# Kernel tuning notes

Measured on AMD Instinct MI355X. Metric: run time of the kernel, lower is better.

The kernel has to match this reference:

```python
import jax, jax.numpy as jnp
import numpy as np

H_SIZE = 1024
N_HEADS = 16
HEAD_DIM = H_SIZE // N_HEADS
TAU2 = 1.0
LN_EPS = 1e-5


def setup_inputs() -> dict:
    key = jax.random.key(0)
    ks = jax.random.split(key, 12)
    B, S = 2, 1024
    s = 1.0 / np.sqrt(H_SIZE)
    inp = {
        "input": jax.random.normal(ks[0], (B, S, H_SIZE), dtype=jnp.float32),
        "input_mask": jnp.ones((B, S), dtype=jnp.float32),
        # uniform(0,1) noise; converted to Gumbel(0,1) inside reference
        "gumbel": jax.random.uniform(ks[1], (B, N_HEADS, S, S), dtype=jnp.float32,
                                     minval=1e-10, maxval=1.0),
        "Wq": jax.random.normal(ks[2], (H_SIZE, H_SIZE), dtype=jnp.float32) * s,
        "bq": jnp.zeros((H_SIZE,), dtype=jnp.float32),
        "Wk": jax.random.normal(ks[3], (H_SIZE, H_SIZE), dtype=jnp.float32) * s,
        "bk": jnp.zeros((H_SIZE,), dtype=jnp.float32),
        "Wv": jax.random.normal(ks[4], (H_SIZE, H_SIZE), dtype=jnp.float32) * s,
        "bv": jnp.zeros((H_SIZE,), dtype=jnp.float32),
        "Wo": jax.random.normal(ks[5], (H_SIZE, H_SIZE), dtype=jnp.float32) * s,
        "bo": jnp.zeros((H_SIZE,), dtype=jnp.float32),
        "gamma": jnp.ones((H_SIZE,), dtype=jnp.float32),
        "beta": jnp.zeros((H_SIZE,), dtype=jnp.float32),
    }
    return inp


def reference(input, input_mask, gumbel, Wq, bq, Wk, bk, Wv, bv, Wo, bo, gamma, beta):
    B, S, _ = input.shape
    # projections -> [B, H, S, D]
    def proj(W, b):
        y = jnp.einsum('bsh,oh->bso', input, W) + b  # torch Linear: x @ W.T + b
        return y.reshape(B, S, N_HEADS, HEAD_DIM).transpose(0, 2, 1, 3)
    qq = proj(Wq, bq)
    kk = proj(Wk, bk)
    vv = proj(Wv, bv)
    # raw scores (NOTE: original has no 1/sqrt(d) scaling)
    interact = jnp.einsum('bhqd,bhkd->bhqk', qq, kk)
    # gumbel-softmax (soft): softmax((logits + g)/tau)
    g = -jnp.log(-jnp.log(gumbel))
    sto_attn = jax.nn.softmax((interact + g) / TAU2, axis=-1)
    # masking: mask_1 over query dim, mask_2 over key dim
    mask = input_mask[:, None, :, None] * input_mask[:, None, None, :]  # [B,1,S,S]
    attn = sto_attn * mask
    # (dropout p=0 -> identity)
    out = jnp.einsum('bhqk,bhkd->bhqd', attn, vv)
    out = out.transpose(0, 2, 1, 3).reshape(B, S, H_SIZE)
    out = jnp.einsum('bsh,oh->bso', out, Wo) + bo
    # residual + layernorm
    x = out + input
    mu = jnp.mean(x, axis=-1, keepdims=True)
    var = jnp.mean(jnp.square(x - mu), axis=-1, keepdims=True)
    return (x - mu) * jax.lax.rsqrt(var + LN_EPS) * gamma + beta
```

## Files before the change

### kernel.cpp

```cpp
#include <hip/hip_runtime.h>

#define S_LEN 1024
#define HSZ   1024
#define NHEAD 16
#define HD    64
#define BATCH 2
#define MROWS 2048
#define SOFTMAX_M0 50.0f

typedef unsigned short u16;
typedef __attribute__((ext_vector_type(8))) short short8;
typedef __attribute__((ext_vector_type(4))) short short4v;
typedef __attribute__((ext_vector_type(4))) float f32x4;

#define MFMA_BF16(a, b, c) __builtin_amdgcn_mfma_f32_16x16x32_bf16((a), (b), (c), 0, 0, 0)

__device__ __forceinline__ u16 f2bf(float f) {
    union { float f; unsigned u; } c; c.f = f;
    unsigned u = c.u;
    u += 0x7fffu + ((u >> 16) & 1u);
    return (u16)(u >> 16);
}
__device__ __forceinline__ float bf2f(u16 s) {
    union { unsigned u; float f; } c; c.u = ((unsigned)s) << 16;
    return c.f;
}
__device__ __forceinline__ short8 ld8(const u16* p) {
    return *reinterpret_cast<const short8*>(p);
}
__device__ __forceinline__ void gld16(const u16* g, u16* l) {
    __builtin_amdgcn_global_load_lds(
        (const __attribute__((address_space(1))) unsigned int*)g,
        (__attribute__((address_space(3))) unsigned int*)l, 16, 0, 0);
}
__device__ __forceinline__ int frag_off(int row, int cbb) {
    return (((row << 3) | (cbb ^ (row & 7))) << 3);
}

template<int MT>
__device__ __forceinline__ void gemm_tile(const u16* __restrict__ Ag,
                                          const u16* __restrict__ Bg,
                                          int klen, u16* As, u16* Bs,
                                          f32x4 (&acc)[MT][4]) {
    const int tid  = threadIdx.x;
    const int wave = tid >> 6, lane = tid & 63;
    const int lr = lane & 15, grp = lane >> 4;
    const int wm = wave >> 1, wn = wave & 1;

#pragma unroll
    for (int mt = 0; mt < MT; mt++)
#pragma unroll
        for (int nt = 0; nt < 4; nt++)
            acc[mt][nt] = (f32x4){0.f, 0.f, 0.f, 0.f};

    for (int k0 = 0; k0 < klen; k0 += 64) {
        __syncthreads();
#pragma unroll
        for (int j = 0; j < MT; j++) {
            int c = j * 256 + tid, row = c >> 3, cb = (c & 7) ^ (row & 7);
            gld16(Ag + (size_t)row * HSZ + k0 + cb * 8, As + c * 8);
        }
#pragma unroll
        for (int j = 0; j < 4; j++) {
            int c = j * 256 + tid, row = c >> 3, cb = (c & 7) ^ (row & 7);
            gld16(Bg + (size_t)row * HSZ + k0 + cb * 8, Bs + c * 8);
        }
        __syncthreads();

#pragma unroll
        for (int h = 0; h < 2; h++) {
            const int cbb = h * 4 + grp;
            short8 af[MT], bf[4];
#pragma unroll
            for (int mt = 0; mt < MT; mt++)
                af[mt] = ld8(As + frag_off(wm * (MT * 16) + mt * 16 + lr, cbb));
#pragma unroll
            for (int nt = 0; nt < 4; nt++)
                bf[nt] = ld8(Bs + frag_off(wn * 64 + nt * 16 + lr, cbb));
#pragma unroll
            for (int mt = 0; mt < MT; mt++)
#pragma unroll
                for (int nt = 0; nt < 4; nt++)
                    acc[mt][nt] = MFMA_BF16(af[mt], bf[nt], acc[mt][nt]);
        }
    }
}

__global__ __launch_bounds__(256)
void convert_kernel(const float* __restrict__ x,  const float* __restrict__ wq,
                    const float* __restrict__ wk, const float* __restrict__ wv,
                    const float* __restrict__ wo, u16* __restrict__ dst) {
    const int XV = (MROWS * HSZ) / 4;
    const int WV = (HSZ * HSZ) / 4;
    int vid = blockIdx.x * 256 + threadIdx.x;
    const float* src; int off;
    if (vid < XV)            { src = x;  off = vid; }
    else if (vid < XV + WV)  { src = wq; off = vid - XV; }
    else if (vid < XV + 2*WV){ src = wk; off = vid - XV - WV; }
    else if (vid < XV + 3*WV){ src = wv; off = vid - XV - 2*WV; }
    else                     { src = wo; off = vid - XV - 3*WV; }
    float4 v = reinterpret_cast<const float4*>(src)[off];
    ushort4 o;
    o.x = f2bf(v.x); o.y = f2bf(v.y); o.z = f2bf(v.z); o.w = f2bf(v.w);
    reinterpret_cast<ushort4*>(dst)[vid] = o;
}

__global__ __launch_bounds__(256)
void qkv_gemm(const u16* __restrict__ xb,
              const u16* __restrict__ wqb, const u16* __restrict__ wkb,
              const u16* __restrict__ wvb,
              const float* __restrict__ bq, const float* __restrict__ bk,
              const float* __restrict__ bv, const float* __restrict__ mask,
              u16* __restrict__ qout, u16* __restrict__ kout,
              u16* __restrict__ vtout) {
    __shared__ u16 As[64 * 64];
    __shared__ u16 Bs[128 * 64];
    const int ntile = blockIdx.x;
    const int mtile = blockIdx.y;
    const int p  = ntile >> 3;
    const int m0 = mtile * 64;
    const int nw = (ntile & 7) * 128;
    const u16*  W    = (p == 0) ? wqb : (p == 1) ? wkb : wvb;
    const float* bias = (p == 0) ? bq : (p == 1) ? bk : bv;

    f32x4 acc[2][4];
    gemm_tile<2>(xb + (size_t)m0 * HSZ, W + (size_t)nw * HSZ, HSZ, As, Bs, acc);

    const int wave = threadIdx.x >> 6, lane = threadIdx.x & 63;
    const int lr = lane & 15, grp = lane >> 4;
    const int wm = wave >> 1, wn = wave & 1;
#pragma unroll
    for (int mt = 0; mt < 2; mt++)
#pragma unroll
        for (int nt = 0; nt < 4; nt++)
#pragma unroll
            for (int r = 0; r < 4; r++) {
                int m = m0 + wm * 32 + mt * 16 + grp * 4 + r;
                int o = nw + wn * 64 + nt * 16 + lr;
                float val = acc[mt][nt][r] + bias[o];
                int b = m >> 10, s = m & 1023, hh = o >> 6, d = o & 63;
                if (p == 0)
                    qout[(((size_t)(b * NHEAD + hh)) * S_LEN + s) * HD + d] = f2bf(val);
                else if (p == 1)
                    kout[(((size_t)(b * NHEAD + hh)) * S_LEN + s) * HD + d] = f2bf(val);
                else
                    vtout[(((size_t)(b * NHEAD + hh)) * HD + d) * S_LEN + s] =
                        f2bf(val * mask[m]);
            }
}

__global__ __launch_bounds__(256, 4)
void attn_kernel(const u16* __restrict__ qb, const u16* __restrict__ kb,
                 const u16* __restrict__ vt, const float* __restrict__ gumbel,
                 u16* __restrict__ po, float* __restrict__ pl) {
    const int bh   = blockIdx.y;
    const int qt   = blockIdx.x;
    const int half = blockIdx.z;
    const int q0 = qt * 64, kbase = half * 512;
    const int tid = threadIdx.x;
    const int wave = tid >> 6, lane = tid & 63;
    const int lr = lane & 15, grp = lane >> 4;

    const u16* Q = qb + (size_t)bh * S_LEN * HD;
    const u16* K = kb + (size_t)bh * S_LEN * HD;
    const u16* V = vt + (size_t)bh * HD * S_LEN;
    const float* G = gumbel + (size_t)bh * S_LEN * S_LEN;
    const int qw = q0 + wave * 16;

    __shared__ u16 pbuf[4 * 16 * 68];
    u16* pw = pbuf + wave * (16 * 68);

    short8 aq0 = ld8(Q + (size_t)(qw + lr) * HD + grp * 8);
    short8 aq1 = ld8(Q + (size_t)(qw + lr) * HD + 32 + grp * 8);

    f32x4 acco[4];
#pragma unroll
    for (int i = 0; i < 4; i++) acco[i] = (f32x4){0.f, 0.f, 0.f, 0.f};
    float lsum[4] = {0.f, 0.f, 0.f, 0.f};

    const float* Grow[4];
#pragma unroll
    for (int r = 0; r < 4; r++)
        Grow[r] = G + (size_t)(qw + grp * 4 + r) * S_LEN + lr;

    for (int it = 0; it < 8; it++) {
        const int k0 = kbase + it * 64;

        float u[4][4];
#pragma unroll
        for (int kt = 0; kt < 4; kt++)
#pragma unroll
            for (int r = 0; r < 4; r++)
                u[kt][r] = Grow[r][k0 + kt * 16];

        float sc[4][4];
#pragma unroll
        for (int kt = 0; kt < 4; kt++) {
            const u16* kp = K + (size_t)(k0 + kt * 16 + lr) * HD + grp * 8;
            short8 kf0 = ld8(kp);
            short8 kf1 = ld8(kp + 32);
            f32x4 a = (f32x4){0.f, 0.f, 0.f, 0.f};
            a = MFMA_BF16(aq0, kf0, a);
            a = MFMA_BF16(aq1, kf1, a);
#pragma unroll
            for (int r = 0; r < 4; r++) sc[kt][r] = a[r];
        }

#pragma unroll
        for (int kt = 0; kt < 4; kt++)
#pragma unroll
            for (int r = 0; r < 4; r++) {
                float w = -__builtin_amdgcn_rcpf(__logf(u[kt][r]));
                float p = __expf(sc[kt][r] - SOFTMAX_M0) * w;
                lsum[r] += p;
                pw[(grp * 4 + r) * 68 + kt * 16 + lr] = f2bf(p);
            }

        short8 pa[2];
#pragma unroll
        for (int ks = 0; ks < 2; ks++) {
            const u16* pp = pw + lr * 68 + ks * 32 + grp * 8;
            short4v lo = *reinterpret_cast<const short4v*>(pp);
            short4v hi = *reinterpret_cast<const short4v*>(pp + 4);
            pa[ks] = __builtin_shufflevector(lo, hi, 0, 1, 2, 3, 4, 5, 6, 7);
        }

#pragma unroll
        for (int nt = 0; nt < 4; nt++) {
            const u16* vp = V + (size_t)(nt * 16 + lr) * S_LEN + k0 + grp * 8;
#pragma unroll
            for (int ks = 0; ks < 2; ks++)
                acco[nt] = MFMA_BF16(pa[ks], ld8(vp + ks * 32), acco[nt]);
        }
    }

#pragma unroll
    for (int r = 0; r < 4; r++) {
        float s = lsum[r];
#pragma unroll
        for (int off = 1; off < 16; off <<= 1)
            s += __shfl_xor(s, off, 64);
        lsum[r] = s;
    }

    const int qidx = ((half * 32 + bh) * 16 + qt) * 64 + wave * 16 + grp * 4;
    if (lr == 0) {
#pragma unroll
        for (int r = 0; r < 4; r++) pl[qidx + r] = lsum[r];
    }
#pragma unroll
    for (int nt = 0; nt < 4; nt++)
#pragma unroll
        for (int r = 0; r < 4; r++)
            po[(size_t)(qidx + r) * 64 + nt * 16 + lr] = f2bf(acco[nt][r]);
}

__global__ __launch_bounds__(256)
void combine_kernel(const u16* __restrict__ po, const float* __restrict__ pl,
                    const float* __restrict__ mask, u16* __restrict__ ctx) {
    const int qt = blockIdx.x, bh = blockIdx.y;
    const int b = bh >> 4, h = bh & 15;
    const int q = threadIdx.x >> 2;
    const int dc = (threadIdx.x & 3) * 16;
    const int i0 = ((0 * 32 + bh) * 16 + qt) * 64 + q;
    const int i1 = ((1 * 32 + bh) * 16 + qt) * 64 + q;
    float l = pl[i0] + pl[i1];
    float mq = mask[b * S_LEN + qt * 64 + q] / l;
    u16* dst = ctx + ((size_t)(b * S_LEN + qt * 64 + q)) * HSZ + h * 64 + dc;
#pragma unroll
    for (int c = 0; c < 2; c++) {
        short8 a = ld8(po + (size_t)i0 * 64 + dc + c * 8);
        short8 bm = ld8(po + (size_t)i1 * 64 + dc + c * 8);
        short8 o;
#pragma unroll
        for (int j = 0; j < 8; j++)
            o[j] = (short)f2bf((bf2f((u16)a[j]) + bf2f((u16)bm[j])) * mq);
        *reinterpret_cast<short8*>(dst + c * 8) = o;
    }
}

__global__ __launch_bounds__(256)
void oproj_gemm(const u16* __restrict__ A, const u16* __restrict__ W,
                float* __restrict__ part0, float* __restrict__ part1) {
    __shared__ u16 As[64 * 64];
    __shared__ u16 Bs[128 * 64];
    const int ntile = blockIdx.x;
    const int mtile = blockIdx.y;
    const int z     = blockIdx.z;
    const int m0 = mtile * 64, n0 = ntile * 128, koff = z * 512;

    f32x4 acc[2][4];
    gemm_tile<2>(A + (size_t)m0 * HSZ + koff, W + (size_t)n0 * HSZ + koff,
                 512, As, Bs, acc);

    float* dst = z ? part1 : part0;
    const int wave = threadIdx.x >> 6, lane = threadIdx.x & 63;
    const int lr = lane & 15, grp = lane >> 4;
    const int wm = wave >> 1, wn = wave & 1;
#pragma unroll
    for (int mt = 0; mt < 2; mt++)
#pragma unroll
        for (int nt = 0; nt < 4; nt++)
#pragma unroll
            for (int r = 0; r < 4; r++) {
                int m = m0 + wm * 32 + mt * 16 + grp * 4 + r;
                int o = n0 + wn * 64 + nt * 16 + lr;
                dst[(size_t)m * HSZ + o] = acc[mt][nt][r];
            }
}

__global__ __launch_bounds__(256)
void ln_kernel(const float* __restrict__ part0, const float* __restrict__ part1,
               const float* __restrict__ xin, const float* __restrict__ bo,
               const float* __restrict__ gamma, const float* __restrict__ beta,
               float* __restrict__ out) {
    const int row = blockIdx.x;
    const int tid = threadIdx.x;
    const size_t base = (size_t)row * (HSZ / 4);

    float4 p0 = reinterpret_cast<const float4*>(part0)[base + tid];
    float4 p1 = reinterpret_cast<const float4*>(part1)[base + tid];
    float4 xr = reinterpret_cast<const float4*>(xin)[base + tid];
    float4 bb = reinterpret_cast<const float4*>(bo)[tid];
    float4 v;
    v.x = p0.x + p1.x + xr.x + bb.x;
    v.y = p0.y + p1.y + xr.y + bb.y;
    v.z = p0.z + p1.z + xr.z + bb.z;
    v.w = p0.w + p1.w + xr.w + bb.w;

    float s  = v.x + v.y + v.z + v.w;
    float ss = v.x * v.x + v.y * v.y + v.z * v.z + v.w * v.w;
#pragma unroll
    for (int off = 1; off < 64; off <<= 1) {
        s  += __shfl_xor(s, off, 64);
        ss += __shfl_xor(ss, off, 64);
    }
    __shared__ float red[8];
    int wave = tid >> 6, lane = tid & 63;
    if (lane == 0) { red[wave] = s; red[4 + wave] = ss; }
    __syncthreads();
    s  = red[0] + red[1] + red[2] + red[3];
    ss = red[4] + red[5] + red[6] + red[7];
    float mu  = s * (1.f / HSZ);
    float var = ss * (1.f / HSZ) - mu * mu;
    float rstd = rsqrtf(var + 1e-5f);

    float4 g  = reinterpret_cast<const float4*>(gamma)[tid];
    float4 be = reinterpret_cast<const float4*>(beta)[tid];
    float4 o;
    o.x = (v.x - mu) * rstd * g.x + be.x;
    o.y = (v.y - mu) * rstd * g.y + be.y;
    o.z = (v.z - mu) * rstd * g.z + be.z;
    o.w = (v.w - mu) * rstd * g.w + be.w;
    reinterpret_cast<float4*>(out)[base + tid] = o;
}

extern "C" void kernel_launch(void* const* d_in, const int* in_sizes, int n_in,
                              void* d_out, int out_size, void* d_ws, size_t ws_size,
                              hipStream_t stream) {
    (void)in_sizes; (void)n_in; (void)out_size; (void)ws_size;
    const float* x     = (const float*)d_in[0];
    const float* mask  = (const float*)d_in[1];
    const float* gum   = (const float*)d_in[2];
    const float* Wq    = (const float*)d_in[3];
    const float* bq    = (const float*)d_in[4];
    const float* Wk    = (const float*)d_in[5];
    const float* bk    = (const float*)d_in[6];
    const float* Wv    = (const float*)d_in[7];
    const float* bv    = (const float*)d_in[8];
    const float* Wo    = (const float*)d_in[9];
    const float* bo    = (const float*)d_in[10];
    const float* gamma = (const float*)d_in[11];
    const float* beta  = (const float*)d_in[12];
    float* out = (float*)d_out;

    u16* xb  = (u16*)d_ws;
    u16* wqb = xb  + 2097152;
    u16* wkb = wqb + 1048576;
    u16* wvb = wkb + 1048576;
    u16* wob = wvb + 1048576;
    u16* qb  = wob + 1048576;
    u16* kb  = qb  + 2097152;
    u16* vt  = kb  + 2097152;
    u16* ctx = vt  + 2097152;
    float* part0 = (float*)(ctx + 2097152);
    float* pl    = (float*)((char*)part0 + 8388608);
    u16*   po    = xb;
    float* part1 = (float*)xb;

    convert_kernel<<<dim3(6144), dim3(256), 0, stream>>>(x, Wq, Wk, Wv, Wo, xb);
    qkv_gemm<<<dim3(24, 32), dim3(256), 0, stream>>>(xb, wqb, wkb, wvb,
                                                     bq, bk, bv, mask,
                                                     qb, kb, vt);
    attn_kernel<<<dim3(16, 32, 2), dim3(256), 0, stream>>>(qb, kb, vt, gum, po, pl);
    combine_kernel<<<dim3(16, 32), dim3(256), 0, stream>>>(po, pl, mask, ctx);
    oproj_gemm<<<dim3(8, 32, 2), dim3(256), 0, stream>>>(ctx, wob, part0, part1);
    ln_kernel<<<dim3(2048), dim3(256), 0, stream>>>(part0, part1, x, bo,
                                                    gamma, beta, out);
}
```

Baseline: 307.3 us.

## Transpose QK MFMA to vectorize gumbel loads and prefetch next tile

Swaps the MFMA operand order so each lane holds four consecutive keys of a single query row. This lets the gumbel noise be read as float4 vectors instead of strided scalar loads, and the softmax probabilities be written to LDS as packed ushort4. The loop is fully unrolled, and the next iteration's gumbel tile plus the current K and V fragments are loaded before the math so that memory latency overlaps compute. The row-sum reduction shrinks to two shuffles. The cost is higher register pressure from the prefetch buffers and fragment arrays, which could reduce occupancy.

```diff
diff --git a/kernel.cpp b/kernel.cpp
--- a/kernel.cpp
+++ b/kernel.cpp
@@ -164,8 +164,8 @@
     const u16* Q = qb + (size_t)bh * S_LEN * HD;
     const u16* K = kb + (size_t)bh * S_LEN * HD;
     const u16* V = vt + (size_t)bh * HD * S_LEN;
-    const float* G = gumbel + (size_t)bh * S_LEN * S_LEN;
     const int qw = q0 + wave * 16;
+    const float* Gp = gumbel + (size_t)bh * S_LEN * S_LEN + (size_t)(qw + lr) * S_LEN;
 
     __shared__ u16 pbuf[4 * 16 * 68];
     u16* pw = pbuf + wave * (16 * 68);
@@ -176,45 +176,54 @@
     f32x4 acco[4];
 #pragma unroll
     for (int i = 0; i < 4; i++) acco[i] = (f32x4){0.f, 0.f, 0.f, 0.f};
-    float lsum[4] = {0.f, 0.f, 0.f, 0.f};
-
-    const float* Grow[4];
-#pragma unroll
-    for (int r = 0; r < 4; r++)
-        Grow[r] = G + (size_t)(qw + grp * 4 + r) * S_LEN + lr;
-
+    float lsum = 0.f;
+
+    f32x4 gc[4], gn[4];
+#pragma unroll
+    for (int kt = 0; kt < 4; kt++)
+        gc[kt] = *reinterpret_cast<const f32x4*>(Gp + kbase + kt * 16 + grp * 4);
+
+#pragma unroll
     for (int it = 0; it < 8; it++) {
         const int k0 = kbase + it * 64;
 
-        float u[4][4];
-#pragma unroll
-        for (int kt = 0; kt < 4; kt++)
-#pragma unroll
-            for (int r = 0; r < 4; r++)
-                u[kt][r] = Grow[r][k0 + kt * 16];
-
-        float sc[4][4];
+        short8 kf[4][2];
 #pragma unroll
         for (int kt = 0; kt < 4; kt++) {
             const u16* kp = K + (size_t)(k0 + kt * 16 + lr) * HD + grp * 8;
-            short8 kf0 = ld8(kp);
-            short8 kf1 = ld8(kp + 32);
+            kf[kt][0] = ld8(kp);
+            kf[kt][1] = ld8(kp + 32);
+        }
+        short8 vf[4][2];
+#pragma unroll
+        for (int nt = 0; nt < 4; nt++) {
+            const u16* vp = V + (size_t)(nt * 16 + lr) * S_LEN + k0 + grp * 8;
+            vf[nt][0] = ld8(vp);
+            vf[nt][1] = ld8(vp + 32);
+        }
+        if (it < 7) {
+#pragma unroll
+            for (int kt = 0; kt < 4; kt++)
+                gn[kt] = *reinterpret_cast<const f32x4*>(Gp + k0 + 64 + kt * 16 + grp * 4);
+        }
+
+#pragma unroll
+        for (int kt = 0; kt < 4; kt++) {
             f32x4 a = (f32x4){0.f, 0.f, 0.f, 0.f};
-            a = MFMA_BF16(aq0, kf0, a);
-            a = MFMA_BF16(aq1, kf1, a);
-#pragma unroll
-            for (int r = 0; r < 4; r++) sc[kt][r] = a[r];
-        }
-
-#pragma unroll
-        for (int kt = 0; kt < 4; kt++)
+            a = MFMA_BF16(kf[kt][0], aq0, a);
+            a = MFMA_BF16(kf[kt][1], aq1, a);
+            float p[4];
 #pragma unroll
             for (int r = 0; r < 4; r++) {
-                float w = -__builtin_amdgcn_rcpf(__logf(u[kt][r]));
-                float p = __expf(sc[kt][r] - SOFTMAX_M0) * w;
-                lsum[r] += p;
-                pw[(grp * 4 + r) * 68 + kt * 16 + lr] = f2bf(p);
+                float w = -__builtin_amdgcn_rcpf(__logf(gc[kt][r]));
+                p[r] = __expf(a[r] - SOFTMAX_M0) * w;
+                lsum += p[r];
             }
+            ushort4 pk;
+            pk.x = f2bf(p[0]); pk.y = f2bf(p[1]);
+            pk.z = f2bf(p[2]); pk.w = f2bf(p[3]);
+            *reinterpret_cast<ushort4*>(pw + lr * 68 + kt * 16 + grp * 4) = pk;
+        }
 
         short8 pa[2];
 #pragma unroll
@@ -226,28 +235,22 @@
         }
 
 #pragma unroll
-        for (int nt = 0; nt < 4; nt++) {
-            const u16* vp = V + (size_t)(nt * 16 + lr) * S_LEN + k0 + grp * 8;
+        for (int nt = 0; nt < 4; nt++)
 #pragma unroll
             for (int ks = 0; ks < 2; ks++)
-                acco[nt] = MFMA_BF16(pa[ks], ld8(vp + ks * 32), acco[nt]);
-        }
+                acco[nt] = MFMA_BF16(pa[ks], vf[nt][ks], acco[nt]);
+
+#pragma unroll
+        for (int kt = 0; kt < 4; kt++) gc[kt] = gn[kt];
     }
 
-#pragma unroll
-    for (int r = 0; r < 4; r++) {
-        float s = lsum[r];
-#pragma unroll
-        for (int off = 1; off < 16; off <<= 1)
-            s += __shfl_xor(s, off, 64);
-        lsum[r] = s;
-    }
-
-    const int qidx = ((half * 32 + bh) * 16 + qt) * 64 + wave * 16 + grp * 4;
-    if (lr == 0) {
-#pragma unroll
-        for (int r = 0; r < 4; r++) pl[qidx + r] = lsum[r];
-    }
+    lsum += __shfl_xor(lsum, 16, 64);
+    lsum += __shfl_xor(lsum, 32, 64);
+
+    const int qbase = ((half * 32 + bh) * 16 + qt) * 64 + wave * 16;
+    if (lane < 16) pl[qbase + lane] = lsum;
+
+    const int qidx = qbase + grp * 4;
 #pragma unroll
     for (int nt = 0; nt < 4; nt++)
 #pragma unroll
```

Result: slower. 335.4 us (+9.1%).
